# Performance work log

Hardware: AMD Instinct MI355X
Metric: run time of the kernel (lower is better)

## Reference

```python
import jax, jax.numpy as jnp
import numpy as np

EMBED_DIM = 1024
NUM_HEADS = 16
HEAD_DIM = EMBED_DIM // NUM_HEADS
SEQ = 2048
BSZ = 2


def setup_inputs() -> dict:
    key = jax.random.key(0)
    ks = jax.random.split(key, 12)
    f = jnp.float32
    query = jax.random.normal(ks[0], (SEQ, BSZ, EMBED_DIM), f)
    k_in = jax.random.normal(ks[1], (SEQ, BSZ, EMBED_DIM), f)
    v_in = jax.random.normal(ks[2], (SEQ, BSZ, EMBED_DIM), f)
    s = 0.02  # weight init scale
    q_w = jax.random.normal(ks[3], (EMBED_DIM, EMBED_DIM), f) * s
    q_b = jax.random.normal(ks[4], (EMBED_DIM,), f) * s
    k_w = jax.random.normal(ks[5], (EMBED_DIM, EMBED_DIM), f) * s
    k_b = jax.random.normal(ks[6], (EMBED_DIM,), f) * s
    v_w = jax.random.normal(ks[7], (EMBED_DIM, EMBED_DIM), f) * s
    v_b = jax.random.normal(ks[8], (EMBED_DIM,), f) * s
    o_w_mean = jax.random.normal(ks[9], (EMBED_DIM, EMBED_DIM), f) * s
    # lgstd ~ uniform(2*log(stdv), log(stdv)) with stdv = 1/sqrt(out+1)
    stdv = 1.0 / np.sqrt(EMBED_DIM + 1)
    o_w_lgstd = jax.random.uniform(ks[10], (EMBED_DIM, EMBED_DIM), f,
                                   2.0 * np.log(stdv), np.log(stdv))
    eps = jax.random.normal(ks[11], (EMBED_DIM, EMBED_DIM), f) * 1.5  # N(0, 1.5)
    return dict(query=query, key=k_in, value=v_in,
                q_w=q_w, q_b=q_b, k_w=k_w, k_b=k_b, v_w=v_w, v_b=v_b,
                o_w_mean=o_w_mean, o_w_lgstd=o_w_lgstd, eps=eps)


def reference(query, key, value, q_w, q_b, k_w, k_b, v_w, v_b,
              o_w_mean, o_w_lgstd, eps):
    tgt_len, bsz, embed_dim = query.shape
    scaling = HEAD_DIM ** -0.5
    # projections (F.linear: x @ W.T + b)
    q = (query @ q_w.T + q_b) * scaling          # [S,B,E]
    k = key @ k_w.T + k_b                        # [S,B,E]
    v = value @ v_w.T + v_b                      # [S,B,E]
    # [S,B,E] -> [B*H, S, hd]
    def split_heads(x, L):
        return x.reshape(L, bsz * NUM_HEADS, HEAD_DIM).transpose(1, 0, 2)
    q = split_heads(q, tgt_len)
    k = split_heads(k, key.shape[0])
    v = split_heads(v, value.shape[0])
    src_len = k.shape[1]
    scores = jnp.einsum('bqd,bkd->bqk', q, k)    # [B*H, S, S] (explicit O(n^2))
    attn = jax.nn.softmax(scores, axis=-1)
    ctx = jnp.einsum('bqk,bkd->bqd', attn, v)    # [B*H, S, hd]
    ctx = ctx.transpose(1, 0, 2).reshape(tgt_len, bsz, embed_dim)
    # Bayesian output projection: sampled weight (training mode), no bias
    o_w = o_w_mean + eps * jnp.exp(o_w_lgstd)
    out = ctx @ o_w.T                            # [S,B,E]
    avg_attn = attn.reshape(bsz, NUM_HEADS, tgt_len, src_len).sum(axis=1) / NUM_HEADS
    return out, avg_attn
```

## Files before the change

kernel.cpp:

```cpp
#include <hip/hip_runtime.h>

#define SQ 2048
#define BB 2
#define EE 1024
#define HH 16
#define DD 64
#define MM (SQ*BB)
#define NSLICE 4
#define KSLICE (SQ/NSLICE)
#define KT_IN (KSLICE/128)
#define LOG2E 1.44269504f

typedef _Float16 f16;
typedef _Float16 half8 __attribute__((ext_vector_type(8)));
typedef _Float16 half4 __attribute__((ext_vector_type(4)));
typedef float f32x4 __attribute__((ext_vector_type(4)));

static __device__ __forceinline__ f32x4 mfma16(half8 a, half8 b, f32x4 c) {
    return __builtin_amdgcn_mfma_f32_16x16x32_f16(a, b, c, 0, 0, 0);
}

static __device__ __forceinline__ void gload16(const f16* g, f16* l) {
    __builtin_amdgcn_global_load_lds(
        (const __attribute__((address_space(1))) unsigned int*)g,
        (__attribute__((address_space(3))) unsigned int*)l, 16, 0, 0);
}

__global__ void k_elem(const float* __restrict__ q_w, const float* __restrict__ k_w,
                       const float* __restrict__ v_w, const float* __restrict__ query,
                       const float* __restrict__ key, const float* __restrict__ value,
                       const float* __restrict__ owm, const float* __restrict__ owl,
                       const float* __restrict__ eps,
                       f16* qw16, f16* kw16, f16* vw16,
                       f16* xq16, f16* xk16, f16* xv16, f16* ow16)
{
    int y = blockIdx.y;
    size_t i = ((size_t)blockIdx.x * 256 + threadIdx.x) * 4;
    if (y < 3) {
        if (i >= (size_t)EE*EE) return;
        const float* s = (y==0) ? q_w : (y==1) ? k_w : v_w;
        f16* d = (y==0) ? qw16 : (y==1) ? kw16 : vw16;
        float4 v = *(const float4*)&s[i];
        half4 o = {(f16)v.x, (f16)v.y, (f16)v.z, (f16)v.w};
        *(half4*)&d[i] = o;
    } else if (y < 6) {
        const float* s = (y==3) ? query : (y==4) ? key : value;
        f16* d = (y==3) ? xq16 : (y==4) ? xk16 : xv16;
        float4 v = *(const float4*)&s[i];
        half4 o = {(f16)v.x, (f16)v.y, (f16)v.z, (f16)v.w};
        *(half4*)&d[i] = o;
    } else {
        if (i >= (size_t)EE*EE) return;
        float4 m = *(const float4*)&owm[i];
        float4 l = *(const float4*)&owl[i];
        float4 e = *(const float4*)&eps[i];
        half4 o = {(f16)(m.x + e.x * __expf(l.x)), (f16)(m.y + e.y * __expf(l.y)),
                   (f16)(m.z + e.z * __expf(l.z)), (f16)(m.w + e.w * __expf(l.w))};
        *(half4*)&ow16[i] = o;
    }
}

__device__ __forceinline__ void gemm_body(
    const f16* __restrict__ A, const f16* __restrict__ W,
    const float* __restrict__ bias, float scale, void* __restrict__ out, int mode)
{
    __shared__ f16 As[128*32];
    __shared__ f16 Bs[64*32];
    int t = threadIdx.x, lane = t & 63, w = t >> 6;
    int quad = lane >> 4, m16 = lane & 15;
    int wm = w >> 1, wn = w & 1;
    int gm0 = blockIdx.x * 128, gn0 = blockIdx.y * 64;
    int arow = lane >> 2, apch = lane & 3;
    f32x4 acc[4][2] = {};
    for (int kt = 0; kt < EE; kt += 32) {
        #pragma unroll
        for (int j = 0; j < 2; ++j) {
            int row = w*32 + j*16 + arow;
            int lch = apch ^ (row & 3);
            gload16(&A[(size_t)(gm0+row)*EE + kt + lch*8], &As[row*32 + apch*8]);
        }
        {
            int row = w*16 + arow;
            int lch = apch ^ (row & 3);
            gload16(&W[(size_t)(gn0+row)*EE + kt + lch*8], &Bs[row*32 + apch*8]);
        }
        __syncthreads();
        int cs = (quad ^ (m16 & 3)) * 8;
        half8 af[4], bf[2];
        #pragma unroll
        for (int i = 0; i < 4; ++i) af[i] = *(half8*)&As[(wm*64 + i*16 + m16)*32 + cs];
        #pragma unroll
        for (int j = 0; j < 2; ++j) bf[j] = *(half8*)&Bs[(wn*32 + j*16 + m16)*32 + cs];
        #pragma unroll
        for (int i = 0; i < 4; ++i)
            #pragma unroll
            for (int j = 0; j < 2; ++j)
                acc[i][j] = mfma16(af[i], bf[j], acc[i][j]);
        __syncthreads();
    }
    #pragma unroll
    for (int j = 0; j < 2; ++j) {
        int col = gn0 + wn*32 + j*16 + m16;
        int h = col >> 6, d = col & 63;
        float bb = bias ? bias[col] : 0.0f;
        #pragma unroll
        for (int i = 0; i < 4; ++i) {
            int r0 = gm0 + wm*64 + i*16 + quad*4;
            #pragma unroll
            for (int r = 0; r < 4; ++r) {
                float v = (acc[i][j][r] + bb) * scale;
                int m = r0 + r;
                int s = m >> 1, b = m & 1;
                if (mode == 2)
                    ((float*)out)[(size_t)m*EE + col] = v;
                else if (mode == 1)
                    ((f16*)out)[((((size_t)b*HH + h)*(SQ/32) + (s >> 5))*DD + d)*32 + (s & 31)] = (f16)v;
                else
                    ((f16*)out)[(((size_t)b*HH + h)*SQ + s)*DD + d] = (f16)v;
            }
        }
    }
}

__global__ __launch_bounds__(256) void k_gemm_qkv(
    const f16* xq, const f16* qw, const float* qb,
    const f16* xk, const f16* kw, const float* kb,
    const f16* xv, const f16* vw, const float* vb,
    f16* Q16, f16* K16, f16* Vt16)
{
    int z = blockIdx.z;
    const f16* A = (z==0) ? xq : (z==1) ? xk : xv;
    const f16* W = (z==0) ? qw : (z==1) ? kw : vw;
    const float* bi = (z==0) ? qb : (z==1) ? kb : vb;
    float sc = (z==0) ? 0.125f * LOG2E : 1.0f;
    void* o = (z==0) ? (void*)Q16 : (z==1) ? (void*)K16 : (void*)Vt16;
    gemm_body(A, W, bi, sc, o, (z==2) ? 1 : 0);
}

__global__ __launch_bounds__(256) void k_gemm_o(const f16* A, const f16* W, float* out)
{
    gemm_body(A, W, nullptr, 1.0f, out, 2);
}

__global__ __launch_bounds__(256, 4) void k_attn_l(
    const f16* __restrict__ Q16, const f16* __restrict__ K16, float* __restrict__ lse2)
{
    __shared__ float red[4][64];
    const int t = threadIdx.x, lane = t & 63, w = t >> 6;
    const int quad = lane >> 4, m16 = lane & 15;
    const int q0 = blockIdx.x * 64, h = blockIdx.y, b = blockIdx.z;
    const f16* Qh = Q16 + ((size_t)b*HH + h)*SQ*DD;
    const f16* Kh = K16 + ((size_t)b*HH + h)*SQ*DD;

    half8 bq[4][2];
    #pragma unroll
    for (int nt = 0; nt < 4; ++nt)
        #pragma unroll
        for (int dk = 0; dk < 2; ++dk)
            bq[nt][dk] = *(const half8*)&Qh[(q0 + nt*16 + m16)*DD + dk*32 + quad*8];

    float lsum[4] = {};
    for (int kt = 0; kt < 16; ++kt) {
        half8 ak[2][2];
        #pragma unroll
        for (int mt = 0; mt < 2; ++mt)
            #pragma unroll
            for (int dk = 0; dk < 2; ++dk)
                ak[mt][dk] = *(const half8*)&Kh[(kt*128 + w*32 + mt*16 + m16)*DD + dk*32 + quad*8];
        #pragma unroll
        for (int mt = 0; mt < 2; ++mt)
            #pragma unroll
            for (int nt = 0; nt < 4; ++nt) {
                f32x4 s = {};
                s = mfma16(ak[mt][0], bq[nt][0], s);
                s = mfma16(ak[mt][1], bq[nt][1], s);
                lsum[nt] += __builtin_amdgcn_exp2f(s[0]) + __builtin_amdgcn_exp2f(s[1])
                          + __builtin_amdgcn_exp2f(s[2]) + __builtin_amdgcn_exp2f(s[3]);
            }
    }
    #pragma unroll
    for (int nt = 0; nt < 4; ++nt) {
        float v = lsum[nt];
        v += __shfl_xor(v, 16, 64);
        v += __shfl_xor(v, 32, 64);
        lsum[nt] = v;
    }
    if (quad == 0)
        #pragma unroll
        for (int nt = 0; nt < 4; ++nt) red[w][nt*16 + m16] = lsum[nt];
    __syncthreads();
    if (t < 64) {
        float v = red[0][t] + red[1][t] + red[2][t] + red[3][t];
        lse2[((size_t)b*HH + h)*SQ + q0 + t] = __log2f(v);
    }
}

__global__ __launch_bounds__(256, 2) void k_attn_main(
    const f16* __restrict__ Q16, const f16* __restrict__ K16, const f16* __restrict__ Vt16,
    const float* __restrict__ lse2, float* __restrict__ ctxp, float* __restrict__ avg_out)
{
    __shared__ f16 ps[2][32][136];
    __shared__ float csh[HH][32];
    const int t = threadIdx.x, lane = t & 63, w = t >> 6;
    const int quad = lane >> 4, m16 = lane & 15;
    const int q0 = blockIdx.x * 32, sl = blockIdx.y, b = blockIdx.z;
    const int ks0 = sl * KSLICE;

    for (int i = t; i < HH*32; i += 256) {
        int hh = i >> 5, qq = i & 31;
        csh[hh][qq] = lse2[((size_t)b*HH + hh)*SQ + q0 + qq];
    }
    __syncthreads();

    float avg_r[KT_IN][16] = {};

    for (int hp = 0; hp < 8; ++hp) {
        f32x4 acc[2][2] = {};
        for (int hh2 = 0; hh2 < 2; ++hh2) {
            const int h = hp*2 + hh2;
            const f16* Qh = Q16 + ((size_t)b*HH + h)*SQ*DD;
            const f16* Kh = K16 + ((size_t)b*HH + h)*SQ*DD;
            const f16* Vh = Vt16 + ((size_t)b*HH + h)*(SQ/32)*DD*32;
            half8 bq[2][2];
            #pragma unroll
            for (int nt = 0; nt < 2; ++nt)
                #pragma unroll
                for (int dk = 0; dk < 2; ++dk)
                    bq[nt][dk] = *(const half8*)&Qh[(q0 + nt*16 + m16)*DD + dk*32 + quad*8];
            const float c01[2] = { csh[h][m16], csh[h][16 + m16] };

            half8 ak[2][2][2], bv[2][4];
            #pragma unroll
            for (int mt = 0; mt < 2; ++mt)
                #pragma unroll
                for (int dk = 0; dk < 2; ++dk)
                    ak[0][mt][dk] = *(const half8*)&Kh[(ks0 + w*32 + mt*16 + m16)*DD + dk*32 + quad*8];
            #pragma unroll
            for (int ks = 0; ks < 4; ++ks)
                bv[0][ks] = *(const half8*)&Vh[(((ks0 + ks*32) >> 5)*DD + w*16 + m16)*32 + quad*8];

            #pragma unroll
            for (int kt = 0; kt < KT_IN; ++kt) {
                const int cur = kt & 1, nxt = cur ^ 1;
                if (kt + 1 < KT_IN) {
                    #pragma unroll
                    for (int mt = 0; mt < 2; ++mt)
                        #pragma unroll
                        for (int dk = 0; dk < 2; ++dk)
                            ak[nxt][mt][dk] = *(const half8*)&Kh[(ks0 + (kt+1)*128 + w*32 + mt*16 + m16)*DD + dk*32 + quad*8];
                    #pragma unroll
                    for (int ks = 0; ks < 4; ++ks)
                        bv[nxt][ks] = *(const half8*)&Vh[(((ks0 + (kt+1)*128 + ks*32) >> 5)*DD + w*16 + m16)*32 + quad*8];
                }
                #pragma unroll
                for (int mt = 0; mt < 2; ++mt)
                    #pragma unroll
                    for (int nt = 0; nt < 2; ++nt) {
                        f32x4 s = {};
                        s = mfma16(ak[cur][mt][0], bq[nt][0], s);
                        s = mfma16(ak[cur][mt][1], bq[nt][1], s);
                        half4 ph;
                        #pragma unroll
                        for (int r = 0; r < 4; ++r) {
                            float p = __builtin_amdgcn_exp2f(s[r] - c01[nt]);
                            avg_r[kt][mt*8 + nt*4 + r] += p;
                            ph[r] = (f16)p;
                        }
                        *(half4*)&ps[cur][nt*16 + m16][w*32 + mt*16 + quad*4] = ph;
                    }
                __builtin_amdgcn_sched_barrier(0);
                __builtin_amdgcn_s_waitcnt(0xC07F);
                __builtin_amdgcn_s_barrier();
                __builtin_amdgcn_sched_barrier(0);
                #pragma unroll
                for (int qt = 0; qt < 2; ++qt) {
                    f32x4 c4 = acc[hh2][qt];
                    #pragma unroll
                    for (int ks = 0; ks < 4; ++ks) {
                        half8 ap = *(half8*)&ps[cur][qt*16 + m16][ks*32 + quad*8];
                        c4 = mfma16(ap, bv[cur][ks], c4);
                    }
                    acc[hh2][qt] = c4;
                }
            }
        }
        #pragma unroll
        for (int hh2 = 0; hh2 < 2; ++hh2)
            #pragma unroll
            for (int qt = 0; qt < 2; ++qt)
                #pragma unroll
                for (int r = 0; r < 4; ++r) {
                    int q = q0 + qt*16 + quad*4 + r;
                    ctxp[(size_t)sl*MM*EE + ((size_t)q*BB + b)*EE + (hp*2 + hh2)*DD + w*16 + m16] = acc[hh2][qt][r];
                }
    }
    #pragma unroll
    for (int kt = 0; kt < KT_IN; ++kt)
        #pragma unroll
        for (int mt = 0; mt < 2; ++mt)
            #pragma unroll
            for (int nt = 0; nt < 2; ++nt) {
                int q = q0 + nt*16 + m16;
                int k = ks0 + kt*128 + w*32 + mt*16 + quad*4;
                float4 v = { avg_r[kt][mt*8+nt*4+0]*(1.0f/HH), avg_r[kt][mt*8+nt*4+1]*(1.0f/HH),
                             avg_r[kt][mt*8+nt*4+2]*(1.0f/HH), avg_r[kt][mt*8+nt*4+3]*(1.0f/HH) };
                *(float4*)&avg_out[((size_t)b*SQ + q)*SQ + k] = v;
            }
}

__global__ void k_ctx_red(const float* __restrict__ ctxp, f16* __restrict__ ctx16) {
    size_t i = ((size_t)blockIdx.x * 256 + threadIdx.x) * 4;
    float4 s = *(const float4*)&ctxp[i];
    #pragma unroll
    for (int sl = 1; sl < NSLICE; ++sl) {
        float4 v = *(const float4*)&ctxp[(size_t)sl*MM*EE + i];
        s.x += v.x; s.y += v.y; s.z += v.z; s.w += v.w;
    }
    half4 o = {(f16)s.x, (f16)s.y, (f16)s.z, (f16)s.w};
    *(half4*)&ctx16[i] = o;
}

extern "C" void kernel_launch(void* const* d_in, const int* in_sizes, int n_in,
                              void* d_out, int out_size, void* d_ws, size_t ws_size,
                              hipStream_t stream) {
    const float* query    = (const float*)d_in[0];
    const float* key      = (const float*)d_in[1];
    const float* value    = (const float*)d_in[2];
    const float* q_w      = (const float*)d_in[3];
    const float* q_b      = (const float*)d_in[4];
    const float* k_w      = (const float*)d_in[5];
    const float* k_b      = (const float*)d_in[6];
    const float* v_w      = (const float*)d_in[7];
    const float* v_b      = (const float*)d_in[8];
    const float* o_w_mean = (const float*)d_in[9];
    const float* o_w_lgstd= (const float*)d_in[10];
    const float* eps      = (const float*)d_in[11];
    float* out = (float*)d_out;
    float* avg = out + (size_t)MM * EE;

    const size_t EWN = (size_t)EE*EE;
    const size_t XWN = (size_t)MM*EE;
    f16* qw16  = (f16*)d_ws;
    f16* kw16  = qw16 + EWN;
    f16* vw16  = kw16 + EWN;
    f16* ow16  = vw16 + EWN;
    f16* Q16   = ow16 + EWN;
    f16* K16   = Q16  + XWN;
    f16* Vt16  = K16  + XWN;
    f16* ctx16 = Vt16 + XWN;
    float* lse2 = (float*)(ctx16 + XWN);
    f16* xq16  = (f16*)(lse2 + (size_t)BB*HH*SQ);
    f16* xk16  = xq16 + XWN;
    f16* xv16  = xk16 + XWN;
    float* ctxp = (float*)xq16;

    k_elem<<<dim3(XWN/1024, 7), 256, 0, stream>>>(q_w, k_w, v_w, query, key, value,
        o_w_mean, o_w_lgstd, eps, qw16, kw16, vw16, xq16, xk16, xv16, ow16);

    k_gemm_qkv<<<dim3(MM/128, EE/64, 3), 256, 0, stream>>>(
        xq16, qw16, q_b, xk16, kw16, k_b, xv16, vw16, v_b, Q16, K16, Vt16);

    k_attn_l   <<<dim3(SQ/64, HH, BB), 256, 0, stream>>>(Q16, K16, lse2);
    k_attn_main<<<dim3(SQ/32, NSLICE, BB), 256, 0, stream>>>(Q16, K16, Vt16, lse2, ctxp, avg);
    k_ctx_red  <<<XWN/1024, 256, 0, stream>>>(ctxp, ctx16);

    k_gemm_o<<<dim3(MM/128, EE/64), 256, 0, stream>>>(ctx16, ow16, out);
}
```

Baseline: 371.5 us.

## Retile attention to 128-query blocks with 16 key slices and fragment-major Q/K layout

Q and K are now stored in a 16x32 MFMA fragment-major layout. The main attention kernel is retiled so each block handles 128 queries by a 128-key slice across all heads, with a single-buffered shared P tile and two barriers per head. Blocks are remapped over a flat grid so neighbouring (slice, batch) groups land on the same XCD. Context partials are written in fp16 across 16 slices, which cuts per-partial bytes but doubles the total reduction traffic, lowers accumulation precision, and may need more workspace than before.

```diff
diff --git a/kernel.cpp b/kernel.cpp
--- a/kernel.cpp
+++ b/kernel.cpp
@@ -6,9 +6,9 @@
 #define HH 16
 #define DD 64
 #define MM (SQ*BB)
-#define NSLICE 4
+#define QT 128
+#define NSLICE 16
 #define KSLICE (SQ/NSLICE)
-#define KT_IN (KSLICE/128)
 #define LOG2E 1.44269504f
 
 typedef _Float16 f16;
@@ -24,6 +24,10 @@
     __builtin_amdgcn_global_load_lds(
         (const __attribute__((address_space(1))) unsigned int*)g,
         (__attribute__((address_space(3))) unsigned int*)l, 16, 0, 0);
+}
+
+static __device__ __forceinline__ size_t qk_frag(size_t bh, int s, int d) {
+    return ((bh*(SQ/16) + (s >> 4))*2 + (d >> 5))*512 + (size_t)(s & 15)*32 + (d & 31);
 }
 
 __global__ void k_elem(const float* __restrict__ q_w, const float* __restrict__ k_w,
@@ -116,7 +120,7 @@
                 else if (mode == 1)
                     ((f16*)out)[((((size_t)b*HH + h)*(SQ/32) + (s >> 5))*DD + d)*32 + (s & 31)] = (f16)v;
                 else
-                    ((f16*)out)[(((size_t)b*HH + h)*SQ + s)*DD + d] = (f16)v;
+                    ((f16*)out)[qk_frag((size_t)b*HH + h, s, d)] = (f16)v;
             }
         }
     }
@@ -145,32 +149,37 @@
 __global__ __launch_bounds__(256, 4) void k_attn_l(
     const f16* __restrict__ Q16, const f16* __restrict__ K16, float* __restrict__ lse2)
 {
-    __shared__ float red[4][64];
+    __shared__ float red[4][128];
     const int t = threadIdx.x, lane = t & 63, w = t >> 6;
     const int quad = lane >> 4, m16 = lane & 15;
-    const int q0 = blockIdx.x * 64, h = blockIdx.y, b = blockIdx.z;
-    const f16* Qh = Q16 + ((size_t)b*HH + h)*SQ*DD;
-    const f16* Kh = K16 + ((size_t)b*HH + h)*SQ*DD;
-
-    half8 bq[4][2];
-    #pragma unroll
-    for (int nt = 0; nt < 4; ++nt)
+    const int bid = blockIdx.x;
+    const int xcd = bid & 7, idx = bid >> 3;
+    const int c = ((idx & 3) << 3) + xcd;
+    const int q0 = (idx >> 2) * 128;
+    const int h = c >> 1, b = c & 1;
+    const size_t bh = (size_t)b*HH + h;
+    const f16* Qf = Q16 + bh*SQ*DD;
+    const f16* Kf = K16 + bh*SQ*DD;
+
+    half8 bq[8][2];
+    #pragma unroll
+    for (int nt = 0; nt < 8; ++nt)
         #pragma unroll
         for (int dk = 0; dk < 2; ++dk)
-            bq[nt][dk] = *(const half8*)&Qh[(q0 + nt*16 + m16)*DD + dk*32 + quad*8];
-
-    float lsum[4] = {};
+            bq[nt][dk] = *(const half8*)&Qf[(((size_t)(q0 >> 4) + nt)*2 + dk)*512 + m16*32 + quad*8];
+
+    float lsum[8] = {};
     for (int kt = 0; kt < 16; ++kt) {
         half8 ak[2][2];
         #pragma unroll
         for (int mt = 0; mt < 2; ++mt)
             #pragma unroll
             for (int dk = 0; dk < 2; ++dk)
-                ak[mt][dk] = *(const half8*)&Kh[(kt*128 + w*32 + mt*16 + m16)*DD + dk*32 + quad*8];
+                ak[mt][dk] = *(const half8*)&Kf[(((size_t)kt*8 + w*2 + mt)*2 + dk)*512 + m16*32 + quad*8];
         #pragma unroll
         for (int mt = 0; mt < 2; ++mt)
             #pragma unroll
-            for (int nt = 0; nt < 4; ++nt) {
+            for (int nt = 0; nt < 8; ++nt) {
                 f32x4 s = {};
                 s = mfma16(ak[mt][0], bq[nt][0], s);
                 s = mfma16(ak[mt][1], bq[nt][1], s);
@@ -179,7 +188,7 @@
             }
     }
     #pragma unroll
-    for (int nt = 0; nt < 4; ++nt) {
+    for (int nt = 0; nt < 8; ++nt) {
         float v = lsum[nt];
         v += __shfl_xor(v, 16, 64);
         v += __shfl_xor(v, 32, 64);
@@ -187,137 +196,140 @@
     }
     if (quad == 0)
         #pragma unroll
-        for (int nt = 0; nt < 4; ++nt) red[w][nt*16 + m16] = lsum[nt];
+        for (int nt = 0; nt < 8; ++nt) red[w][nt*16 + m16] = lsum[nt];
     __syncthreads();
-    if (t < 64) {
+    if (t < 128) {
         float v = red[0][t] + red[1][t] + red[2][t] + red[3][t];
-        lse2[((size_t)b*HH + h)*SQ + q0 + t] = __log2f(v);
+        lse2[bh*SQ + q0 + t] = __log2f(v);
     }
 }
 
 __global__ __launch_bounds__(256, 2) void k_attn_main(
     const f16* __restrict__ Q16, const f16* __restrict__ K16, const f16* __restrict__ Vt16,
-    const float* __restrict__ lse2, float* __restrict__ ctxp, float* __restrict__ avg_out)
-{
-    __shared__ f16 ps[2][32][136];
-    __shared__ float csh[HH][32];
+    const float* __restrict__ lse2, f16* __restrict__ ctxp, float* __restrict__ avg_out)
+{
+    __shared__ f16 ps[128][136];
+    __shared__ float csh[HH][QT];
     const int t = threadIdx.x, lane = t & 63, w = t >> 6;
     const int quad = lane >> 4, m16 = lane & 15;
-    const int q0 = blockIdx.x * 32, sl = blockIdx.y, b = blockIdx.z;
+    const int bid = blockIdx.x;
+    const int xcd = bid & 7, idx = bid >> 3;
+    const int c = ((idx & 3) << 3) + xcd;
+    const int q0 = (idx >> 2) * QT;
+    const int sl = c >> 1, b = c & 1;
     const int ks0 = sl * KSLICE;
 
-    for (int i = t; i < HH*32; i += 256) {
-        int hh = i >> 5, qq = i & 31;
-        csh[hh][qq] = lse2[((size_t)b*HH + hh)*SQ + q0 + qq];
-    }
+    for (int i = t; i < HH*QT; i += 256)
+        csh[i >> 7][i & 127] = lse2[((size_t)b*HH + (i >> 7))*SQ + q0 + (i & 127)];
     __syncthreads();
 
-    float avg_r[KT_IN][16] = {};
-
-    for (int hp = 0; hp < 8; ++hp) {
-        f32x4 acc[2][2] = {};
-        for (int hh2 = 0; hh2 < 2; ++hh2) {
-            const int h = hp*2 + hh2;
-            const f16* Qh = Q16 + ((size_t)b*HH + h)*SQ*DD;
-            const f16* Kh = K16 + ((size_t)b*HH + h)*SQ*DD;
-            const f16* Vh = Vt16 + ((size_t)b*HH + h)*(SQ/32)*DD*32;
-            half8 bq[2][2];
-            #pragma unroll
-            for (int nt = 0; nt < 2; ++nt)
-                #pragma unroll
-                for (int dk = 0; dk < 2; ++dk)
-                    bq[nt][dk] = *(const half8*)&Qh[(q0 + nt*16 + m16)*DD + dk*32 + quad*8];
-            const float c01[2] = { csh[h][m16], csh[h][16 + m16] };
-
-            half8 ak[2][2][2], bv[2][4];
-            #pragma unroll
-            for (int mt = 0; mt < 2; ++mt)
-                #pragma unroll
-                for (int dk = 0; dk < 2; ++dk)
-                    ak[0][mt][dk] = *(const half8*)&Kh[(ks0 + w*32 + mt*16 + m16)*DD + dk*32 + quad*8];
-            #pragma unroll
-            for (int ks = 0; ks < 4; ++ks)
-                bv[0][ks] = *(const half8*)&Vh[(((ks0 + ks*32) >> 5)*DD + w*16 + m16)*32 + quad*8];
-
-            #pragma unroll
-            for (int kt = 0; kt < KT_IN; ++kt) {
-                const int cur = kt & 1, nxt = cur ^ 1;
-                if (kt + 1 < KT_IN) {
+    float avg_r[8][8] = {};
+
+    for (int h = 0; h < HH; ++h) {
+        const size_t bh = (size_t)b*HH + h;
+        const f16* Qf = Q16 + bh*SQ*DD;
+        const f16* Kf = K16 + bh*SQ*DD;
+        const f16* Vh = Vt16 + bh*SQ*DD;
+
+        half8 ak[2][2];
+        #pragma unroll
+        for (int mt = 0; mt < 2; ++mt)
+            #pragma unroll
+            for (int dk = 0; dk < 2; ++dk)
+                ak[mt][dk] = *(const half8*)&Kf[(((size_t)(ks0 >> 4) + w*2 + mt)*2 + dk)*512 + m16*32 + quad*8];
+        half8 bv[4];
+        #pragma unroll
+        for (int ks = 0; ks < 4; ++ks)
+            bv[ks] = *(const half8*)&Vh[(((size_t)(ks0 >> 5) + ks)*DD + w*16 + m16)*32 + quad*8];
+
+        half8 bqA[2], bqB[2];
+        #pragma unroll
+        for (int dk = 0; dk < 2; ++dk)
+            bqA[dk] = *(const half8*)&Qf[(((size_t)(q0 >> 4) + 0)*2 + dk)*512 + m16*32 + quad*8];
+        #pragma unroll
+        for (int nt = 0; nt < 8; ++nt) {
+            if (nt + 1 < 8) {
+                if (nt & 1) {
                     #pragma unroll
-                    for (int mt = 0; mt < 2; ++mt)
-                        #pragma unroll
-                        for (int dk = 0; dk < 2; ++dk)
-                            ak[nxt][mt][dk] = *(const half8*)&Kh[(ks0 + (kt+1)*128 + w*32 + mt*16 + m16)*DD + dk*32 + quad*8];
+                    for (int dk = 0; dk < 2; ++dk)
+                        bqA[dk] = *(const half8*)&Qf[(((size_t)(q0 >> 4) + nt + 1)*2 + dk)*512 + m16*32 + quad*8];
+                } else {
                     #pragma unroll
-                    for (int ks = 0; ks < 4; ++ks)
-                        bv[nxt][ks] = *(const half8*)&Vh[(((ks0 + (kt+1)*128 + ks*32) >> 5)*DD + w*16 + m16)*32 + quad*8];
+                    for (int dk = 0; dk < 2; ++dk)
+                        bqB[dk] = *(const half8*)&Qf[(((size_t)(q0 >> 4) + nt + 1)*2 + dk)*512 + m16*32 + quad*8];
                 }
-                #pragma unroll
-                for (int mt = 0; mt < 2; ++mt)
-                    #pragma unroll
-                    for (int nt = 0; nt < 2; ++nt) {
-                        f32x4 s = {};
-                        s = mfma16(ak[cur][mt][0], bq[nt][0], s);
-                        s = mfma16(ak[cur][mt][1], bq[nt][1], s);
-                        half4 ph;
-                        #pragma unroll
-                        for (int r = 0; r < 4; ++r) {
-                            float p = __builtin_amdgcn_exp2f(s[r] - c01[nt]);
-                            avg_r[kt][mt*8 + nt*4 + r] += p;
-                            ph[r] = (f16)p;
-                        }
-                        *(half4*)&ps[cur][nt*16 + m16][w*32 + mt*16 + quad*4] = ph;
-                    }
-                __builtin_amdgcn_sched_barrier(0);
-                __builtin_amdgcn_s_waitcnt(0xC07F);
-                __builtin_amdgcn_s_barrier();
-                __builtin_amdgcn_sched_barrier(0);
-                #pragma unroll
-                for (int qt = 0; qt < 2; ++qt) {
-                    f32x4 c4 = acc[hh2][qt];
-                    #pragma unroll
-                    for (int ks = 0; ks < 4; ++ks) {
-                        half8 ap = *(half8*)&ps[cur][qt*16 + m16][ks*32 + quad*8];
-                        c4 = mfma16(ap, bv[cur][ks], c4);
-                    }
-                    acc[hh2][qt] = c4;
+            }
+            const float cc = csh[h][nt*16 + m16];
+            #pragma unroll
+            for (int mt = 0; mt < 2; ++mt) {
+                f32x4 s = {};
+                if (nt & 1) {
+                    s = mfma16(ak[mt][0], bqB[0], s);
+                    s = mfma16(ak[mt][1], bqB[1], s);
+                } else {
+                    s = mfma16(ak[mt][0], bqA[0], s);
+                    s = mfma16(ak[mt][1], bqA[1], s);
                 }
-            }
-        }
-        #pragma unroll
-        for (int hh2 = 0; hh2 < 2; ++hh2)
-            #pragma unroll
-            for (int qt = 0; qt < 2; ++qt)
+                half4 ph;
                 #pragma unroll
                 for (int r = 0; r < 4; ++r) {
-                    int q = q0 + qt*16 + quad*4 + r;
-                    ctxp[(size_t)sl*MM*EE + ((size_t)q*BB + b)*EE + (hp*2 + hh2)*DD + w*16 + m16] = acc[hh2][qt][r];
+                    float p = __builtin_amdgcn_exp2f(s[r] - cc);
+                    avg_r[nt][mt*4 + r] += p;
+                    ph[r] = (f16)p;
                 }
-    }
-    #pragma unroll
-    for (int kt = 0; kt < KT_IN; ++kt)
-        #pragma unroll
-        for (int mt = 0; mt < 2; ++mt)
-            #pragma unroll
-            for (int nt = 0; nt < 2; ++nt) {
-                int q = q0 + nt*16 + m16;
-                int k = ks0 + kt*128 + w*32 + mt*16 + quad*4;
-                float4 v = { avg_r[kt][mt*8+nt*4+0]*(1.0f/HH), avg_r[kt][mt*8+nt*4+1]*(1.0f/HH),
-                             avg_r[kt][mt*8+nt*4+2]*(1.0f/HH), avg_r[kt][mt*8+nt*4+3]*(1.0f/HH) };
-                *(float4*)&avg_out[((size_t)b*SQ + q)*SQ + k] = v;
-            }
-}
-
-__global__ void k_ctx_red(const float* __restrict__ ctxp, f16* __restrict__ ctx16) {
-    size_t i = ((size_t)blockIdx.x * 256 + threadIdx.x) * 4;
-    float4 s = *(const float4*)&ctxp[i];
-    #pragma unroll
-    for (int sl = 1; sl < NSLICE; ++sl) {
-        float4 v = *(const float4*)&ctxp[(size_t)sl*MM*EE + i];
-        s.x += v.x; s.y += v.y; s.z += v.z; s.w += v.w;
-    }
-    half4 o = {(f16)s.x, (f16)s.y, (f16)s.z, (f16)s.w};
-    *(half4*)&ctx16[i] = o;
+                *(half4*)&ps[nt*16 + m16][w*32 + mt*16 + quad*4] = ph;
+            }
+        }
+        __builtin_amdgcn_sched_barrier(0);
+        __builtin_amdgcn_s_waitcnt(0xC07F);
+        __builtin_amdgcn_s_barrier();
+        __builtin_amdgcn_sched_barrier(0);
+
+        #pragma unroll
+        for (int qt = 0; qt < 8; ++qt) {
+            f32x4 cacc = {};
+            #pragma unroll
+            for (int ks = 0; ks < 4; ++ks) {
+                half8 ap = *(half8*)&ps[qt*16 + m16][ks*32 + quad*8];
+                cacc = mfma16(ap, bv[ks], cacc);
+            }
+            #pragma unroll
+            for (int r = 0; r < 4; ++r) {
+                int q = q0 + qt*16 + quad*4 + r;
+                ctxp[(size_t)sl*MM*EE + ((size_t)q*BB + b)*EE + h*DD + w*16 + m16] = (f16)cacc[r];
+            }
+        }
+        __builtin_amdgcn_sched_barrier(0);
+        __builtin_amdgcn_s_waitcnt(0xC07F);
+        __builtin_amdgcn_s_barrier();
+        __builtin_amdgcn_sched_barrier(0);
+    }
+
+    #pragma unroll
+    for (int nt = 0; nt < 8; ++nt)
+        #pragma unroll
+        for (int mt = 0; mt < 2; ++mt) {
+            int q = q0 + nt*16 + m16;
+            int k = ks0 + w*32 + mt*16 + quad*4;
+            float4 v = { avg_r[nt][mt*4+0]*(1.0f/HH), avg_r[nt][mt*4+1]*(1.0f/HH),
+                         avg_r[nt][mt*4+2]*(1.0f/HH), avg_r[nt][mt*4+3]*(1.0f/HH) };
+            *(float4*)&avg_out[((size_t)b*SQ + q)*SQ + k] = v;
+        }
+}
+
+__global__ void k_ctx_red(const f16* __restrict__ ctxp, f16* __restrict__ ctx16) {
+    size_t i = ((size_t)blockIdx.x * 256 + threadIdx.x) * 8;
+    float s[8] = {};
+    #pragma unroll
+    for (int sl = 0; sl < NSLICE; ++sl) {
+        half8 v = *(const half8*)&ctxp[(size_t)sl*MM*EE + i];
+        #pragma unroll
+        for (int j = 0; j < 8; ++j) s[j] += (float)v[j];
+    }
+    half8 o;
+    #pragma unroll
+    for (int j = 0; j < 8; ++j) o[j] = (f16)s[j];
+    *(half8*)&ctx16[i] = o;
 }
 
 extern "C" void kernel_launch(void* const* d_in, const int* in_sizes, int n_in,
@@ -352,7 +364,7 @@
     f16* xq16  = (f16*)(lse2 + (size_t)BB*HH*SQ);
     f16* xk16  = xq16 + XWN;
     f16* xv16  = xk16 + XWN;
-    float* ctxp = (float*)xq16;
+    f16* ctxp = xq16;
 
     k_elem<<<dim3(XWN/1024, 7), 256, 0, stream>>>(q_w, k_w, v_w, query, key, value,
         o_w_mean, o_w_lgstd, eps, qw16, kw16, vw16, xq16, xk16, xv16, ow16);
@@ -360,9 +372,9 @@
     k_gemm_qkv<<<dim3(MM/128, EE/64, 3), 256, 0, stream>>>(
         xq16, qw16, q_b, xk16, kw16, k_b, xv16, vw16, v_b, Q16, K16, Vt16);
 
-    k_attn_l   <<<dim3(SQ/64, HH, BB), 256, 0, stream>>>(Q16, K16, lse2);
-    k_attn_main<<<dim3(SQ/32, NSLICE, BB), 256, 0, stream>>>(Q16, K16, Vt16, lse2, ctxp, avg);
-    k_ctx_red  <<<XWN/1024, 256, 0, stream>>>(ctxp, ctx16);
+    k_attn_l   <<<dim3((SQ/128) * HH * BB), 256, 0, stream>>>(Q16, K16, lse2);
+    k_attn_main<<<dim3((SQ/QT) * NSLICE * BB), 256, 0, stream>>>(Q16, K16, Vt16, lse2, ctxp, avg);
+    k_ctx_red  <<<XWN/2048, 256, 0, stream>>>(ctxp, ctx16);
 
     k_gemm_o<<<dim3(MM/128, EE/64), 256, 0, stream>>>(ctx16, ow16, out);
 }
```

After: 333.4 us. 1.11x faster.
